# Kernel tuning notes

Measured on AMD Instinct MI355X. Metric: run time of the kernel, lower is better.

## Reference

```python
import jax, jax.numpy as jnp
import numpy as np

RADIUS = 6
KSIZE = 2 * RADIUS + 1  # 13


def setup_inputs() -> dict:
    key = jax.random.key(0)
    k1, k2 = jax.random.split(key)
    B, C, H, W = 8, 256, 128, 128
    z_t = jax.random.normal(k1, (B, C, H, W), dtype=jnp.float32)
    z_t1 = jax.random.normal(k2, (B, C, H, W), dtype=jnp.float32)
    return {"z_t": z_t, "z_t1": z_t1}


def reference(z_t, z_t1):
    B, C, H, W = z_t.shape
    r, K = RADIUS, KSIZE
    # zero-pad neighbor frame spatially (matches F.unfold padding=radius)
    zp = jnp.pad(z_t1, ((0, 0), (0, 0), (r, r), (r, r)))
    # kernel tap offsets in torch-unfold order: index k = i*K + j (row-major)
    ii, jj = jnp.meshgrid(jnp.arange(K), jnp.arange(K), indexing="ij")
    offsets = jnp.stack([ii.reshape(-1), jj.reshape(-1)], axis=-1)  # [K*K, 2]

    def tap(carry, off):
        # window: padded[:, :, i:i+H, j:j+W]  == z_t1 shifted by (i-r, j-r)
        win = jax.lax.dynamic_slice(zp, (0, 0, off[0], off[1]), (B, C, H, W))
        s = jnp.einsum("bchw,bchw->bhw", z_t, win)  # channel dot per pixel
        return carry, s

    _, scores = jax.lax.scan(tap, None, offsets)  # [K*K, B, H, W]
    scores = jnp.transpose(scores, (1, 0, 2, 3))  # [B, K*K, H, W]
    return scores / jnp.sqrt(jnp.asarray(C, dtype=z_t.dtype))
```

## Files before the change

kernel.cpp:

```cpp
#include <hip/hip_runtime.h>
#include <hip/hip_bf16.h>


#define CC 256
#define HH 128
#define WW 128
#define NT 169
#define PH 8
#define PW 16
#define QH 20
#define QW 28
#define CCH 32
#define NCH 8
#define CS 40
#define NPIXB (QH*QW)
#define NPIXA (PH*PW)
#define NUB (NPIXB*4)
#define NUNIT (NUB + NPIXA*4)
#define UPT 6
#define CHPLANE (HH*WW)
#define ABYTE (NPIXB*CS*2)
#define KHALF 85
#define OSTRIDE 132

typedef __attribute__((ext_vector_type(8))) short bf16x8;
typedef __attribute__((ext_vector_type(4))) float f32x4;

union SMEM {
    unsigned short stage[NPIXB*CS + NPIXA*CS];
    float outb[KHALF*OSTRIDE];
};

static __device__ __forceinline__ unsigned pk2(float a, float b) {
    unsigned x = __bfloat16_as_ushort(__float2bfloat16(a));
    unsigned y = __bfloat16_as_ushort(__float2bfloat16(b));
    return x | (y << 16);
}

__global__ __launch_bounds__(512, 2)
void lc_mfma(const float* __restrict__ zt, const float* __restrict__ zt1,
             float* __restrict__ out) {
    __shared__ SMEM sm;
    char* smb = (char*)&sm;

    const int tid  = threadIdx.x;
    const int lane = tid & 63;
    const int wid  = tid >> 6;
    const int py0  = (wid >> 2) * 4;
    const int px0  = (wid & 3) * 4;

    const int bid = blockIdx.x;
    const int b   = bid & 7;
    const int t   = bid >> 3;
    const int h0  = (t >> 3) * PH;
    const int w0  = (t & 7) * PW;

    const float* src[UPT];
    int   dstB[UPT];
    bool  ex[UPT], pv[UPT];
#pragma unroll
    for (int v = 0; v < UPT; ++v) {
        const int ui = tid + v * 512;
        ex[v] = ui < NUNIT;
        int pix, oct, gy, gx, valid;
        const float* base;
        if (ui < NUB) {
            oct = ui / NPIXB;
            pix = ui - oct * NPIXB;
            const int qyi = pix / QW;
            const int qxi = pix - qyi * QW;
            gy = h0 + qyi - 6;
            gx = w0 + qxi - 6;
            valid = (gy >= 0) & (gy < HH) & (gx >= 0) & (gx < WW);
            base = zt1;
            dstB[v] = pix * (CS*2) + oct * 16;
        } else {
            const int u2 = ui - NUB;
            oct = u2 >> 7;
            pix = u2 & 127;
            gy = h0 + (pix >> 4);
            gx = w0 + (pix & 15);
            valid = 1;
            base = zt;
            dstB[v] = ABYTE + pix * (CS*2) + oct * 16;
        }
        pv[v] = valid;
        src[v] = base + (((b * CC + oct * 8) * HH + (valid ? gy : 0)) * WW + (valid ? gx : 0));
    }

    const int nlo = lane & 3, nhi = (lane >> 2) & 3, oo = lane >> 4;
    int boff[16];
#pragma unroll
    for (int qi = 0; qi < 16; ++qi) {
        const int qyL = py0 + (qi >> 2) * 4 + nhi;
        const int qxL = px0 + (qi & 3) * 4 + nlo;
        boff[qi] = (qyL * QW + qxL) * (CS*2) + oo * 16;
    }
    const int pixA = (py0 + nhi) * PW + px0 + nlo;
    const int aoff = ABYTE + pixA * (CS*2) + oo * 16;

    f32x4 acc[16];
#pragma unroll
    for (int qi = 0; qi < 16; ++qi) acc[qi] = (f32x4){0.f, 0.f, 0.f, 0.f};

    float pf[UPT][8];
#pragma unroll
    for (int v = 0; v < UPT; ++v) {
        const bool ld = ex[v] && pv[v];
#pragma unroll
        for (int j = 0; j < 8; ++j) pf[v][j] = ld ? src[v][j * CHPLANE] : 0.f;
        src[v] += CCH * CHPLANE;
    }

    for (int kc = 0; kc < NCH; ++kc) {
#pragma unroll
        for (int v = 0; v < UPT; ++v) {
            if (ex[v]) {
                uint4 q;
                q.x = pk2(pf[v][0], pf[v][1]);
                q.y = pk2(pf[v][2], pf[v][3]);
                q.z = pk2(pf[v][4], pf[v][5]);
                q.w = pk2(pf[v][6], pf[v][7]);
                *(uint4*)(smb + dstB[v]) = q;
            }
        }
        if (kc + 1 < NCH) {
#pragma unroll
            for (int v = 0; v < UPT; ++v) {
                const bool ld = ex[v] && pv[v];
#pragma unroll
                for (int j = 0; j < 8; ++j) pf[v][j] = ld ? src[v][j * CHPLANE] : 0.f;
                src[v] += CCH * CHPLANE;
            }
        }
        __syncthreads();

        const bf16x8 af = *(const bf16x8*)(smb + aoff);
#pragma unroll
        for (int qi = 0; qi < 16; ++qi) {
            const bf16x8 bfr = *(const bf16x8*)(smb + boff[qi]);
            acc[qi] = __builtin_amdgcn_mfma_f32_16x16x32_bf16(af, bfr, acc[qi], 0, 0, 0);
        }
        __syncthreads();
    }

    const int psb = (py0 + oo) * PW + px0;
#pragma unroll 1
    for (int pass = 0; pass < 2; ++pass) {
        const int kb = pass * KHALF;
        const int nk = pass ? (NT - KHALF) : KHALF;
#pragma unroll
        for (int qi = 0; qi < 16; ++qi) {
            const int di = 4 * (qi >> 2) + nhi - oo;
            const bool diok = (unsigned)di <= 12u;
            const int dib = di * 13;
#pragma unroll
            for (int r = 0; r < 4; ++r) {
                const int dj = 4 * (qi & 3) + nlo - r;
                const int k  = dib + dj;
                if (diok && (unsigned)dj <= 12u && k >= kb && k < kb + nk)
                    sm.outb[(k - kb) * OSTRIDE + psb + r] = acc[qi][r] * 0.0625f;
            }
        }
        __syncthreads();
        const int total4 = nk * 32;
        for (int i = tid; i < total4; i += 512) {
            const int row = i >> 5, j = i & 31;
            const float4 val = *(const float4*)&sm.outb[row * OSTRIDE + j * 4];
            float* dst = out + (((b * NT + kb + row) * HH + h0 + (j >> 2)) * WW
                                + w0 + (j & 3) * 4);
            *(float4*)dst = val;
        }
        __syncthreads();
    }
}

extern "C" void kernel_launch(void* const* d_in, const int* in_sizes, int n_in,
                              void* d_out, int out_size, void* d_ws, size_t ws_size,
                              hipStream_t stream) {
    const float* zt  = (const float*)d_in[0];
    const float* zt1 = (const float*)d_in[1];
    float* out = (float*)d_out;
    lc_mfma<<<dim3(1024), dim3(512), 0, stream>>>(zt, zt1, out);
}
```

Measured before the change: 143.5 us.

## Double-buffer LDS staging, use 1024-thread blocks, load float2 pairs

Raises the block to 1024 threads (16 waves), with each wave computing half of the shifted-window MFMA tiles. This halves per-wave accumulator registers and adds wave-level parallelism. LDS staging is now double-buffered, so the next channel chunk is written while the current one is consumed, removing one barrier per chunk. Global loads fetch two adjacent pixels per thread as float2, cutting load instruction count. The larger LDS footprint and thread count may limit blocks per CU.

```diff
diff --git a/kernel.cpp b/kernel.cpp
--- a/kernel.cpp
+++ b/kernel.cpp
@@ -6,28 +6,25 @@
 #define HH 128
 #define WW 128
 #define NT 169
-#define PH 8
 #define PW 16
-#define QH 20
-#define QW 28
-#define CCH 32
-#define NCH 8
-#define CS 40
-#define NPIXB (QH*QW)
-#define NPIXA (PH*PW)
-#define NUB (NPIXB*4)
-#define NUNIT (NUB + NPIXA*4)
-#define UPT 6
+#define QWD 28
+#define PIXB 80
+#define NPB 560
+#define NPA 128
+#define BBUF (NPB*PIXB)
+#define ABUF (NPA*PIXB)
 #define CHPLANE (HH*WW)
-#define ABYTE (NPIXB*CS*2)
+#define CHUNK_ADV (32*CHPLANE)
 #define KHALF 85
 #define OSTRIDE 132
+#define NBU 1120
+#define NAU 256
 
 typedef __attribute__((ext_vector_type(8))) short bf16x8;
 typedef __attribute__((ext_vector_type(4))) float f32x4;
 
 union SMEM {
-    unsigned short stage[NPIXB*CS + NPIXA*CS];
+    char raw[2*BBUF + 2*ABUF];
     float outb[KHALF*OSTRIDE];
 };
 
@@ -37,138 +34,145 @@
     return x | (y << 16);
 }
 
-__global__ __launch_bounds__(512, 2)
-void lc_mfma(const float* __restrict__ zt, const float* __restrict__ zt1,
-             float* __restrict__ out) {
+__global__ __launch_bounds__(1024, 4)
+void lc_mfma2(const float* __restrict__ zt, const float* __restrict__ zt1,
+              float* __restrict__ out) {
     __shared__ SMEM sm;
-    char* smb = (char*)&sm;
+    char* smb = sm.raw;
 
     const int tid  = threadIdx.x;
     const int lane = tid & 63;
     const int wid  = tid >> 6;
-    const int py0  = (wid >> 2) * 4;
-    const int px0  = (wid & 3) * 4;
+    const int pw   = wid & 7;
+    const int qh   = wid >> 3;
+    const int py0  = (pw >> 2) * 4;
+    const int px0  = (pw & 3) * 4;
+    const int nlo  = lane & 3, nhi = (lane >> 2) & 3, oo = lane >> 4;
 
     const int bid = blockIdx.x;
     const int b   = bid & 7;
     const int t   = bid >> 3;
-    const int h0  = (t >> 3) * PH;
+    const int h0  = (t >> 3) * 8;
     const int w0  = (t & 7) * PW;
 
-    const float* src[UPT];
-    int   dstB[UPT];
-    bool  ex[UPT], pv[UPT];
+    const float* usrc[2];
+    int udst[2], usel[2];
+    bool uval[2], uact[2];
 #pragma unroll
-    for (int v = 0; v < UPT; ++v) {
-        const int ui = tid + v * 512;
-        ex[v] = ui < NUNIT;
-        int pix, oct, gy, gx, valid;
-        const float* base;
-        if (ui < NUB) {
-            oct = ui / NPIXB;
-            pix = ui - oct * NPIXB;
-            const int qyi = pix / QW;
-            const int qxi = pix - qyi * QW;
-            gy = h0 + qyi - 6;
-            gx = w0 + qxi - 6;
-            valid = (gy >= 0) & (gy < HH) & (gx >= 0) & (gx < WW);
-            base = zt1;
-            dstB[v] = pix * (CS*2) + oct * 16;
-        } else {
-            const int u2 = ui - NUB;
-            oct = u2 >> 7;
-            pix = u2 & 127;
-            gy = h0 + (pix >> 4);
-            gx = w0 + (pix & 15);
-            valid = 1;
-            base = zt;
-            dstB[v] = ABYTE + pix * (CS*2) + oct * 16;
+    for (int s = 0; s < 2; ++s) {
+        const int u = tid + s * 1024;
+        const bool actB = u < NBU;
+        const bool actA = (u >= NBU) && (u < NBU + NAU);
+        uact[s] = actB || actA;
+        int dst = 0, sel = 0;
+        bool val = false;
+        const float* src = zt1;
+        if (actA) {
+            const int u2 = u - NBU;
+            const int oct = u2 >> 6, pp = u2 & 63;
+            const int py = pp >> 3, pxp = pp & 7;
+            dst = (py*16 + pxp*2) * PIXB + oct*16;
+            sel = 1; val = true;
+            src = zt + (((size_t)(b*CC + oct*8) * HH + (h0 + py)) * WW + (w0 + pxp*2));
+        } else if (actB) {
+            const int oct = u / 280, pp = u % 280;
+            const int qy = pp / 14, qxp = pp % 14;
+            const int gy = h0 + qy - 6, gx = w0 + qxp*2 - 6;
+            val = (gy >= 0) && (gy < HH) && (gx >= 0) && (gx < WW);
+            dst = (qy*QWD + qxp*2) * PIXB + oct*16;
+            sel = 0;
+            src = zt1 + (((size_t)(b*CC + oct*8) * HH + (val ? gy : 0)) * WW + (val ? gx : 0));
         }
-        pv[v] = valid;
-        src[v] = base + (((b * CC + oct * 8) * HH + (valid ? gy : 0)) * WW + (valid ? gx : 0));
+        uval[s] = val; udst[s] = dst; usel[s] = sel; usrc[s] = src;
     }
 
-    const int nlo = lane & 3, nhi = (lane >> 2) & 3, oo = lane >> 4;
-    int boff[16];
+    const int laneBoff = ((py0 + nhi)*QWD + (px0 + nlo))*PIXB + oo*16 + qh*17920;
+    const int laneAoff = 2*BBUF + ((py0 + nhi)*PW + (px0 + nlo))*PIXB + oo*16;
+
+    f32x4 acc[8];
 #pragma unroll
-    for (int qi = 0; qi < 16; ++qi) {
-        const int qyL = py0 + (qi >> 2) * 4 + nhi;
-        const int qxL = px0 + (qi & 3) * 4 + nlo;
-        boff[qi] = (qyL * QW + qxL) * (CS*2) + oo * 16;
-    }
-    const int pixA = (py0 + nhi) * PW + px0 + nlo;
-    const int aoff = ABYTE + pixA * (CS*2) + oo * 16;
+    for (int j = 0; j < 8; ++j) acc[j] = (f32x4){0.f, 0.f, 0.f, 0.f};
 
-    f32x4 acc[16];
-#pragma unroll
-    for (int qi = 0; qi < 16; ++qi) acc[qi] = (f32x4){0.f, 0.f, 0.f, 0.f};
+    float pfx[2][8], pfy[2][8];
 
-    float pf[UPT][8];
-#pragma unroll
-    for (int v = 0; v < UPT; ++v) {
-        const bool ld = ex[v] && pv[v];
-#pragma unroll
-        for (int j = 0; j < 8; ++j) pf[v][j] = ld ? src[v][j * CHPLANE] : 0.f;
-        src[v] += CCH * CHPLANE;
+#define STAGE_LOAD(KC)                                                        \
+    _Pragma("unroll")                                                         \
+    for (int s = 0; s < 2; ++s) {                                             \
+        if (uact[s]) {                                                        \
+            const float* p = usrc[s] + (size_t)(KC) * CHUNK_ADV;              \
+            const bool v = uval[s];                                           \
+            _Pragma("unroll")                                                 \
+            for (int j = 0; j < 8; ++j) {                                     \
+                float2 d = v ? *(const float2*)(p + j*CHPLANE)                \
+                             : make_float2(0.f, 0.f);                         \
+                pfx[s][j] = d.x; pfy[s][j] = d.y;                             \
+            }                                                                 \
+        }                                                                     \
     }
 
-    for (int kc = 0; kc < NCH; ++kc) {
+#define STAGE_WRITE(PAR)                                                      \
+    _Pragma("unroll")                                                         \
+    for (int s = 0; s < 2; ++s) {                                             \
+        if (uact[s]) {                                                        \
+            const int base = usel[s] ? (2*BBUF + (PAR)*ABUF) : ((PAR)*BBUF);  \
+            uint4 q0, q1;                                                     \
+            q0.x = pk2(pfx[s][0], pfx[s][1]); q0.y = pk2(pfx[s][2], pfx[s][3]);\
+            q0.z = pk2(pfx[s][4], pfx[s][5]); q0.w = pk2(pfx[s][6], pfx[s][7]);\
+            q1.x = pk2(pfy[s][0], pfy[s][1]); q1.y = pk2(pfy[s][2], pfy[s][3]);\
+            q1.z = pk2(pfy[s][4], pfy[s][5]); q1.w = pk2(pfy[s][6], pfy[s][7]);\
+            *(uint4*)(smb + base + udst[s]) = q0;                             \
+            *(uint4*)(smb + base + udst[s] + PIXB) = q1;                      \
+        }                                                                     \
+    }
+
+    STAGE_LOAD(0)
+    STAGE_WRITE(0)
+    __syncthreads();
+
 #pragma unroll
-        for (int v = 0; v < UPT; ++v) {
-            if (ex[v]) {
-                uint4 q;
-                q.x = pk2(pf[v][0], pf[v][1]);
-                q.y = pk2(pf[v][2], pf[v][3]);
-                q.z = pk2(pf[v][4], pf[v][5]);
-                q.w = pk2(pf[v][6], pf[v][7]);
-                *(uint4*)(smb + dstB[v]) = q;
-            }
+    for (int kc = 0; kc < 8; ++kc) {
+        if (kc + 1 < 8) { STAGE_LOAD(kc + 1) }
+
+        const char* bbase = smb + (kc & 1)*BBUF + laneBoff;
+        const char* abase = smb + (kc & 1)*ABUF + laneAoff;
+        const bf16x8 af = *(const bf16x8*)abase;
+#pragma unroll
+        for (int j = 0; j < 8; ++j) {
+            const int imm = (j >> 2)*8960 + (j & 3)*320;
+            const bf16x8 bfr = *(const bf16x8*)(bbase + imm);
+            acc[j] = __builtin_amdgcn_mfma_f32_16x16x32_bf16(af, bfr, acc[j], 0, 0, 0);
         }
-        if (kc + 1 < NCH) {
-#pragma unroll
-            for (int v = 0; v < UPT; ++v) {
-                const bool ld = ex[v] && pv[v];
-#pragma unroll
-                for (int j = 0; j < 8; ++j) pf[v][j] = ld ? src[v][j * CHPLANE] : 0.f;
-                src[v] += CCH * CHPLANE;
-            }
-        }
-        __syncthreads();
 
-        const bf16x8 af = *(const bf16x8*)(smb + aoff);
-#pragma unroll
-        for (int qi = 0; qi < 16; ++qi) {
-            const bf16x8 bfr = *(const bf16x8*)(smb + boff[qi]);
-            acc[qi] = __builtin_amdgcn_mfma_f32_16x16x32_bf16(af, bfr, acc[qi], 0, 0, 0);
-        }
+        if (kc + 1 < 8) { STAGE_WRITE((kc + 1) & 1) }
         __syncthreads();
     }
 
-    const int psb = (py0 + oo) * PW + px0;
+    const int psb = (py0 + oo)*PW + px0;
 #pragma unroll 1
     for (int pass = 0; pass < 2; ++pass) {
         const int kb = pass * KHALF;
         const int nk = pass ? (NT - KHALF) : KHALF;
 #pragma unroll
-        for (int qi = 0; qi < 16; ++qi) {
-            const int di = 4 * (qi >> 2) + nhi - oo;
+        for (int jj = 0; jj < 8; ++jj) {
+            const int qi = qh*8 + jj;
+            const int di = 4*(qi >> 2) + nhi - oo;
             const bool diok = (unsigned)di <= 12u;
             const int dib = di * 13;
 #pragma unroll
             for (int r = 0; r < 4; ++r) {
-                const int dj = 4 * (qi & 3) + nlo - r;
+                const int dj = 4*(qi & 3) + nlo - r;
                 const int k  = dib + dj;
                 if (diok && (unsigned)dj <= 12u && k >= kb && k < kb + nk)
-                    sm.outb[(k - kb) * OSTRIDE + psb + r] = acc[qi][r] * 0.0625f;
+                    sm.outb[(k - kb)*OSTRIDE + psb + r] = acc[jj][r] * 0.0625f;
             }
         }
         __syncthreads();
         const int total4 = nk * 32;
-        for (int i = tid; i < total4; i += 512) {
+        for (int i = tid; i < total4; i += 1024) {
             const int row = i >> 5, j = i & 31;
-            const float4 val = *(const float4*)&sm.outb[row * OSTRIDE + j * 4];
-            float* dst = out + (((b * NT + kb + row) * HH + h0 + (j >> 2)) * WW
-                                + w0 + (j & 3) * 4);
+            const float4 val = *(const float4*)&sm.outb[row*OSTRIDE + j*4];
+            float* dst = out + (((size_t)(b*NT + kb + row)*HH + h0 + (j >> 2))*WW
+                                + w0 + (j & 3)*4);
             *(float4*)dst = val;
         }
         __syncthreads();
@@ -181,5 +185,5 @@
     const float* zt  = (const float*)d_in[0];
     const float* zt1 = (const float*)d_in[1];
     float* out = (float*)d_out;
-    lc_mfma<<<dim3(1024), dim3(512), 0, stream>>>(zt, zt1, out);
+    lc_mfma2<<<dim3(1024), dim3(1024), 0, stream>>>(zt, zt1, out);
 }
```

New measurement: 255.5 us. 78.1% more time.

## Pre-transpose neighbor frame to channel-last bf16 and stream via global_load_lds double buffer

Applied to the files above, without the earlier changes.

Adds a pre-pass kernel that converts z_t1 into a channel-last bf16 workspace, with a zeroed pad page standing in for out-of-bounds pixels. The main kernel then loads halo fragments straight into double-buffered LDS using global_load_lds with an XOR swizzle, and prefetches the A tile one chunk ahead. This removes the strided fp32 gathers and in-register packing for the 20x28 halo, which was re-read by every tile. In exchange it adds a separate launch with an extra full read and write of z_t1 in bf16, and uses more LDS per block.

```diff
diff --git a/kernel.cpp b/kernel.cpp
--- a/kernel.cpp
+++ b/kernel.cpp
@@ -2,149 +2,139 @@
 #include <hip/hip_bf16.h>
 
 
-#define CC 256
-#define HH 128
-#define WW 128
+#define CHPL 16384
 #define NT 169
-#define PH 8
-#define PW 16
-#define QH 20
-#define QW 28
-#define CCH 32
-#define NCH 8
-#define CS 40
-#define NPIXB (QH*QW)
-#define NPIXA (PH*PW)
-#define NUB (NPIXB*4)
-#define NUNIT (NUB + NPIXA*4)
-#define UPT 6
-#define CHPLANE (HH*WW)
-#define ABYTE (NPIXB*CS*2)
 #define KHALF 85
 #define OSTRIDE 132
+#define BFRAG 35840
+#define AFRAG_OFF (2*BFRAG)
+#define SMTOT (AFRAG_OFF + 8192)
 
 typedef __attribute__((ext_vector_type(8))) short bf16x8;
 typedef __attribute__((ext_vector_type(4))) float f32x4;
+typedef unsigned int u32;
+typedef unsigned short u16;
 
-union SMEM {
-    unsigned short stage[NPIXB*CS + NPIXA*CS];
-    float outb[KHALF*OSTRIDE];
-};
-
-static __device__ __forceinline__ unsigned pk2(float a, float b) {
-    unsigned x = __bfloat16_as_ushort(__float2bfloat16(a));
-    unsigned y = __bfloat16_as_ushort(__float2bfloat16(b));
-    return x | (y << 16);
+static __device__ __forceinline__ u32 pk2(float a, float b) {
+    __hip_bfloat162 h = __float22bfloat162_rn(make_float2(a, b));
+    union { __hip_bfloat162 h2; u32 u; } c; c.h2 = h; return c.u;
 }
 
-__global__ __launch_bounds__(512, 2)
-void lc_mfma(const float* __restrict__ zt, const float* __restrict__ zt1,
-             float* __restrict__ out) {
-    __shared__ SMEM sm;
-    char* smb = (char*)&sm;
+__global__ __launch_bounds__(256)
+void lc_tr(const float* __restrict__ zt1, void* __restrict__ ws) {
+    __shared__ float ld[64][68];
+    const int tid = threadIdx.x, bid = blockIdx.x;
+    const int cb = bid & 3, wb = (bid >> 2) & 1;
+    const int h = (bid >> 3) & 127, b = bid >> 10;
+    if (bid == 0 && tid < 128) ((u32*)ws)[tid] = 0u;
+    const int c0 = cb * 64, w0 = wb * 64;
+#pragma unroll
+    for (int k = 0; k < 4; ++k) {
+        const int u = tid + k * 256, ch = u >> 4, seg = u & 15;
+        const float4 v = *(const float4*)(zt1 + ((size_t)(b * 256 + c0 + ch)) * CHPL
+                                          + h * 128 + w0 + seg * 4);
+        *(float4*)&ld[ch][seg * 4] = v;
+    }
+    __syncthreads();
+    const int px = tid >> 2, part = tid & 3;
+    u32 r[8];
+#pragma unroll
+    for (int j = 0; j < 8; ++j)
+        r[j] = pk2(ld[part * 16 + 2 * j][px], ld[part * 16 + 2 * j + 1][px]);
+    u16* dst = (u16*)((char*)ws + 512)
+               + ((size_t)(b * 16384 + h * 128 + w0 + px)) * 256 + c0 + part * 16;
+    *(uint4*)dst = make_uint4(r[0], r[1], r[2], r[3]);
+    *(uint4*)(dst + 8) = make_uint4(r[4], r[5], r[6], r[7]);
+}
 
-    const int tid  = threadIdx.x;
-    const int lane = tid & 63;
-    const int wid  = tid >> 6;
-    const int py0  = (wid >> 2) * 4;
-    const int px0  = (wid & 3) * 4;
+__global__ __launch_bounds__(512, 4)
+void lc9(const float* __restrict__ zt, const void* __restrict__ ws,
+         float* __restrict__ out) {
+    __shared__ union { char raw[SMTOT]; float outb[KHALF * OSTRIDE]; } sm;
+    char* smb = sm.raw;
+    const int tid = threadIdx.x, lane = tid & 63, wid = tid >> 6;
+    const int bid = blockIdx.x;
+    const int b = bid & 7, t = bid >> 3;
+    const int h0 = (t >> 3) * 8, w0 = (t & 7) * 16;
+    const int py0 = (wid >> 2) * 4, px0 = (wid & 3) * 4;
+    const int nlo = lane & 3, nhi = (lane >> 2) & 3, oo = lane >> 4;
 
-    const int bid = blockIdx.x;
-    const int b   = bid & 7;
-    const int t   = bid >> 3;
-    const int h0  = (t >> 3) * PH;
-    const int w0  = (t & 7) * PW;
+    const u16* zw = (const u16*)((const char*)ws + 512);
+    const char* zpg = (const char*)ws;
 
-    const float* src[UPT];
-    int   dstB[UPT];
-    bool  ex[UPT], pv[UPT];
+    const char* bsrc[5]; int badv[5]; int bdst[5];
+    if (wid < 7) {
 #pragma unroll
-    for (int v = 0; v < UPT; ++v) {
-        const int ui = tid + v * 512;
-        ex[v] = ui < NUNIT;
-        int pix, oct, gy, gx, valid;
-        const float* base;
-        if (ui < NUB) {
-            oct = ui / NPIXB;
-            pix = ui - oct * NPIXB;
-            const int qyi = pix / QW;
-            const int qxi = pix - qyi * QW;
-            gy = h0 + qyi - 6;
-            gx = w0 + qxi - 6;
-            valid = (gy >= 0) & (gy < HH) & (gx >= 0) & (gx < WW);
-            base = zt1;
-            dstB[v] = pix * (CS*2) + oct * 16;
-        } else {
-            const int u2 = ui - NUB;
-            oct = u2 >> 7;
-            pix = u2 & 127;
-            gy = h0 + (pix >> 4);
-            gx = w0 + (pix & 15);
-            valid = 1;
-            base = zt;
-            dstB[v] = ABYTE + pix * (CS*2) + oct * 16;
+        for (int i = 0; i < 5; ++i) {
+            const int I = wid * 5 + i;
+            const int g = I * 64 + lane;
+            const int px = g >> 2, slot = g & 3;
+            const int qy = px / 28, qx = px % 28;
+            const int gy = h0 + qy - 6, gx = w0 + qx - 6;
+            const bool val = (gy >= 0) && (gy < 128) && (gx >= 0) && (gx < 128);
+            const int ss = slot ^ ((px >> 1) & 3);
+            bsrc[i] = val ? (const char*)(zw + ((size_t)(b * 16384 + gy * 128 + gx)) * 256
+                                          + ss * 8)
+                          : zpg;
+            badv[i] = val ? 64 : 0;
+            bdst[i] = I * 1024;
         }
-        pv[v] = valid;
-        src[v] = base + (((b * CC + oct * 8) * HH + (valid ? gy : 0)) * WW + (valid ? gx : 0));
     }
 
-    const int nlo = lane & 3, nhi = (lane >> 2) & 3, oo = lane >> 4;
+#define BISSUE(PAR) if (wid < 7) { _Pragma("unroll")                           \
+    for (int i = 0; i < 5; ++i) {                                              \
+        __builtin_amdgcn_global_load_lds(                                      \
+            (const __attribute__((address_space(1))) void*)bsrc[i],            \
+            (__attribute__((address_space(3))) void*)(smb + (PAR)*BFRAG + bdst[i]), \
+            16, 0, 0);                                                         \
+        bsrc[i] += badv[i]; } }
+
+    const int octA = tid >> 7, pxu = tid & 127;
+    const float* asrc = zt + ((size_t)(b * 256 + octA * 8)) * CHPL
+                        + (h0 + (pxu >> 4)) * 128 + w0 + (pxu & 15);
+    const int awoff = AFRAG_OFF + pxu * 64 + ((octA ^ ((pxu >> 1) & 3)) << 4);
+    float pfA[2][8];
+
+#define AISSUE(KC, PAR) { _Pragma("unroll")                                    \
+    for (int e = 0; e < 8; ++e)                                                \
+        pfA[PAR][e] = asrc[((size_t)((KC) * 32 + e)) * CHPL]; }
+
+#define APACK(PAR) { uint4 q;                                                  \
+    q.x = pk2(pfA[PAR][0], pfA[PAR][1]); q.y = pk2(pfA[PAR][2], pfA[PAR][3]);  \
+    q.z = pk2(pfA[PAR][4], pfA[PAR][5]); q.w = pk2(pfA[PAR][6], pfA[PAR][7]);  \
+    *(uint4*)(smb + awoff) = q; }
+
     int boff[16];
 #pragma unroll
     for (int qi = 0; qi < 16; ++qi) {
-        const int qyL = py0 + (qi >> 2) * 4 + nhi;
-        const int qxL = px0 + (qi & 3) * 4 + nlo;
-        boff[qi] = (qyL * QW + qxL) * (CS*2) + oo * 16;
+        const int px = (py0 + (qi >> 2) * 4 + nhi) * 28 + (px0 + (qi & 3) * 4 + nlo);
+        boff[qi] = px * 64 + ((oo ^ ((px >> 1) & 3)) << 4);
     }
-    const int pixA = (py0 + nhi) * PW + px0 + nlo;
-    const int aoff = ABYTE + pixA * (CS*2) + oo * 16;
+    const int pxm = (py0 + nhi) * 16 + px0 + nlo;
+    const int aoff = AFRAG_OFF + pxm * 64 + ((oo ^ ((pxm >> 1) & 3)) << 4);
 
     f32x4 acc[16];
 #pragma unroll
     for (int qi = 0; qi < 16; ++qi) acc[qi] = (f32x4){0.f, 0.f, 0.f, 0.f};
 
-    float pf[UPT][8];
+    BISSUE(0) AISSUE(0, 0)
 #pragma unroll
-    for (int v = 0; v < UPT; ++v) {
-        const bool ld = ex[v] && pv[v];
-#pragma unroll
-        for (int j = 0; j < 8; ++j) pf[v][j] = ld ? src[v][j * CHPLANE] : 0.f;
-        src[v] += CCH * CHPLANE;
-    }
-
-    for (int kc = 0; kc < NCH; ++kc) {
-#pragma unroll
-        for (int v = 0; v < UPT; ++v) {
-            if (ex[v]) {
-                uint4 q;
-                q.x = pk2(pf[v][0], pf[v][1]);
-                q.y = pk2(pf[v][2], pf[v][3]);
-                q.z = pk2(pf[v][4], pf[v][5]);
-                q.w = pk2(pf[v][6], pf[v][7]);
-                *(uint4*)(smb + dstB[v]) = q;
-            }
-        }
-        if (kc + 1 < NCH) {
-#pragma unroll
-            for (int v = 0; v < UPT; ++v) {
-                const bool ld = ex[v] && pv[v];
-#pragma unroll
-                for (int j = 0; j < 8; ++j) pf[v][j] = ld ? src[v][j * CHPLANE] : 0.f;
-                src[v] += CCH * CHPLANE;
-            }
-        }
-        __syncthreads();
-
+    for (int kc = 0; kc < 8; ++kc) {
+        asm volatile("s_waitcnt vmcnt(0)\n\ts_barrier" ::: "memory");
+        if (kc < 7) { BISSUE((kc + 1) & 1) AISSUE(kc + 1, (kc + 1) & 1) }
+        APACK(kc & 1)
+        asm volatile("s_waitcnt lgkmcnt(0)\n\ts_barrier" ::: "memory");
+        const char* fb = smb + (kc & 1) * BFRAG;
         const bf16x8 af = *(const bf16x8*)(smb + aoff);
 #pragma unroll
         for (int qi = 0; qi < 16; ++qi) {
-            const bf16x8 bfr = *(const bf16x8*)(smb + boff[qi]);
+            const bf16x8 bfr = *(const bf16x8*)(fb + boff[qi]);
             acc[qi] = __builtin_amdgcn_mfma_f32_16x16x32_bf16(af, bfr, acc[qi], 0, 0, 0);
         }
-        __syncthreads();
     }
+    __syncthreads();
 
-    const int psb = (py0 + oo) * PW + px0;
+    const int psb = (py0 + oo) * 16 + px0;
 #pragma unroll 1
     for (int pass = 0; pass < 2; ++pass) {
         const int kb = pass * KHALF;
@@ -167,7 +157,7 @@
         for (int i = tid; i < total4; i += 512) {
             const int row = i >> 5, j = i & 31;
             const float4 val = *(const float4*)&sm.outb[row * OSTRIDE + j * 4];
-            float* dst = out + (((b * NT + kb + row) * HH + h0 + (j >> 2)) * WW
+            float* dst = out + (((size_t)(b * NT + kb + row) * 128 + h0 + (j >> 2)) * 128
                                 + w0 + (j & 3) * 4);
             *(float4*)dst = val;
         }
@@ -181,5 +171,6 @@
     const float* zt  = (const float*)d_in[0];
     const float* zt1 = (const float*)d_in[1];
     float* out = (float*)d_out;
-    lc_mfma<<<dim3(1024), dim3(512), 0, stream>>>(zt, zt1, out);
+    lc_tr<<<dim3(8192), dim3(256), 0, stream>>>(zt1, d_ws);
+    lc9<<<dim3(1024), dim3(512), 0, stream>>>(zt, d_ws, out);
 }
```

Result: slower. 148.3 us (+3.4%).
